# Kernel optimization log

Hardware: AMD Instinct MI355X
Metric: run time of the kernel (lower is better)

Reference implementation:

```python
import jax, jax.numpy as jnp
import numpy as np

B, T, N, D = 2, 256, 128, 512
H = 8
D_INNER, D_STATE, D_CONV, DT_RANK = 2 * D, 16, 4, D // 16  # mamba defaults
EPS = 1e-5


def setup_inputs() -> dict:
    key = jax.random.key(0)
    ks = iter(jax.random.split(key, 32))
    g = lambda shape, s=0.02: jax.random.normal(next(ks), shape, dtype=jnp.float32) * s
    return {
        "x": jax.random.normal(next(ks), (B, T, N, D), dtype=jnp.float32),
        "mha_in_w": g((3 * D, D)), "mha_in_b": jnp.zeros((3 * D,), jnp.float32),
        "mha_out_w": g((D, D)), "mha_out_b": jnp.zeros((D,), jnp.float32),
        "n1_w": jnp.ones((D,), jnp.float32),
        "n2_w": jnp.ones((D,), jnp.float32),
        "n3_w": jnp.ones((D,), jnp.float32),
        "m_in_w": g((2 * D_INNER, D)),
        "m_conv_w": g((D_INNER, 1, D_CONV), 0.1), "m_conv_b": jnp.zeros((D_INNER,), jnp.float32),
        "m_xproj_w": g((DT_RANK + 2 * D_STATE, D_INNER)),
        "m_dt_w": g((D_INNER, DT_RANK)), "m_dt_b": jnp.full((D_INNER,), -4.6, jnp.float32),
        "m_A_log": jnp.tile(jnp.log(jnp.arange(1, D_STATE + 1, dtype=jnp.float32)), (D_INNER, 1)),
        "m_D": jnp.ones((D_INNER,), jnp.float32),
        "m_out_w": g((D, D_INNER)),
        "mlp_w1": g((2 * D, D)), "mlp_b1": jnp.zeros((2 * D,), jnp.float32),
        "mlp_w2": g((D, 2 * D)), "mlp_b2": jnp.zeros((D,), jnp.float32),
    }


def rmsnorm(x, w):
    return x * jax.lax.rsqrt(jnp.mean(x * x, axis=-1, keepdims=True) + EPS) * w


def mha(x, in_w, in_b, out_w, out_b):
    # x: (Bt, N, D); torch nn.MultiheadAttention with batch_first=True
    Bt, n, d = x.shape
    dh = d // H
    qkv = x @ in_w.T + in_b
    q, k, v = jnp.split(qkv, 3, axis=-1)
    q = q.reshape(Bt, n, H, dh)
    k = k.reshape(Bt, n, H, dh)
    v = v.reshape(Bt, n, H, dh)
    att = jax.nn.softmax(jnp.einsum('bnhd,bmhd->bhnm', q, k) / jnp.sqrt(jnp.float32(dh)), axis=-1)
    o = jnp.einsum('bhnm,bmhd->bnhd', att, v).reshape(Bt, n, d)
    return o @ out_w.T + out_b


def mamba(x, in_w, conv_w, conv_b, xproj_w, dt_w, dt_b, A_log, Dp, out_w):
    # x: (Bm, L, D)  -- standard mamba_ssm Mamba block (expand=2, d_state=16, d_conv=4)
    Bm, L, _ = x.shape
    xz = x @ in_w.T                      # (Bm, L, 2*d_inner)
    xm, z = jnp.split(xz, 2, axis=-1)
    # causal depthwise conv1d along time
    xc = jnp.pad(xm.transpose(0, 2, 1), ((0, 0), (0, 0), (D_CONV - 1, 0)))
    xc = jax.lax.conv_general_dilated(xc, conv_w, (1,), 'VALID',
                                      dimension_numbers=('NCH', 'OIH', 'NCH'),
                                      feature_group_count=D_INNER)
    xm = jax.nn.silu(xc.transpose(0, 2, 1) + conv_b)   # (Bm, L, d_inner)
    x_dbl = xm @ xproj_w.T
    dt, Bs, Cs = jnp.split(x_dbl, [DT_RANK, DT_RANK + D_STATE], axis=-1)
    dt = jax.nn.softplus(dt @ dt_w.T + dt_b)           # (Bm, L, d_inner)
    A = -jnp.exp(A_log)                                # (d_inner, d_state)

    def step(h, inp):
        dt_t, B_t, C_t, u_t = inp                      # (Bm,d_in),(Bm,ds),(Bm,ds),(Bm,d_in)
        dA = jnp.exp(dt_t[:, :, None] * A)             # (Bm, d_inner, d_state)
        h = dA * h + (dt_t * u_t)[:, :, None] * B_t[:, None, :]
        y = jnp.einsum('bds,bs->bd', h, C_t)
        return h, y

    h0 = jnp.zeros((Bm, D_INNER, D_STATE), x.dtype)
    inputs = (dt.transpose(1, 0, 2), Bs.transpose(1, 0, 2),
              Cs.transpose(1, 0, 2), xm.transpose(1, 0, 2))
    _, ys = jax.lax.scan(step, h0, inputs)
    y = ys.transpose(1, 0, 2) + xm * Dp
    y = y * jax.nn.silu(z)
    return y @ out_w.T


def reference(x, mha_in_w, mha_in_b, mha_out_w, mha_out_b, n1_w, n2_w, n3_w,
              m_in_w, m_conv_w, m_conv_b, m_xproj_w, m_dt_w, m_dt_b, m_A_log, m_D, m_out_w,
              mlp_w1, mlp_b1, mlp_w2, mlp_b2):
    Bx, Tx, Nx, Dx = x.shape
    # spatial attention over regions
    xs = x.reshape(Bx * Tx, Nx, Dx)
    xs = rmsnorm(xs + mha(xs, mha_in_w, mha_in_b, mha_out_w, mha_out_b), n1_w)
    # temporal mamba over time
    xt = xs.reshape(Bx, Tx, Nx, Dx).transpose(0, 2, 1, 3).reshape(Bx * Nx, Tx, Dx)
    xt = rmsnorm(xt + mamba(xt, m_in_w, m_conv_w, m_conv_b, m_xproj_w,
                            m_dt_w, m_dt_b, m_A_log, m_D, m_out_w), n2_w)
    # MLP (1 hidden layer, width 2*D, ReLU)
    x3 = xt.reshape(Bx, Nx, Tx, Dx).transpose(0, 2, 1, 3)
    h = jax.nn.relu(x3 @ mlp_w1.T + mlp_b1) @ mlp_w2.T + mlp_b2
    return rmsnorm(x3 + h, n3_w)
```

## Files before the change

kernel.cpp:

```cpp
#include <hip/hip_runtime.h>

typedef unsigned short u16;
typedef unsigned int u32;
typedef __attribute__((ext_vector_type(8))) short short8;
typedef __attribute__((ext_vector_type(4))) float f32x4;

__device__ __forceinline__ float bf2f(u16 u){ union{u32 i; float f;} v; v.i=((u32)u)<<16; return v.f; }
__device__ __forceinline__ u16 f2bf(float f){ union{float f; u32 i;} v; v.f=f; u32 r=v.i+0x7FFFu+((v.i>>16)&1u); return (u16)(r>>16); }

__device__ __forceinline__ void glds16(const u16* g, u16* lds){
  __builtin_amdgcn_global_load_lds((const __attribute__((address_space(1))) u32*)g,
                                   (__attribute__((address_space(3))) u32*)lds, 16, 0, 0);
}

__global__ __launch_bounds__(256) void cvt_kernel(const float* __restrict__ src, u16* __restrict__ dst, int n4){
  int i = blockIdx.x*256 + threadIdx.x;
  if (i >= n4) return;
  float4 v = ((const float4*)src)[i];
  union { u16 o[4]; uint2 q; } t;
  t.o[0]=f2bf(v.x); t.o[1]=f2bf(v.y); t.o[2]=f2bf(v.z); t.o[3]=f2bf(v.w);
  ((uint2*)dst)[i] = t.q;
}

template<int BM, int BN, int EPI>
__global__ __launch_bounds__(256, 2) void gemm_bt_kernel(
    const u16* __restrict__ A, int lda,
    const u16* __restrict__ B,
    const float* __restrict__ bias,
    u16* __restrict__ C, int ldc,
    int N, int K)
{
  constexpr int RM = BM/32, RN = BN/32;
  constexpr int AI = BM/64, BI = BN/64;
  const int tid = threadIdx.x;
  const int wave = tid>>6, lane = tid&63;
  const int wm = wave>>1, wn = wave&1;
  const int lm = lane&15, quad = lane>>4;
  const int bm0 = blockIdx.x*BM, bn0 = blockIdx.y*BN;
  __shared__ __align__(16) u16 As[BM*32];
  __shared__ __align__(16) u16 Bs[BN*32];
  f32x4 acc[RM][RN] = {};
  const int vr = tid>>2, vc = (tid&3)<<3;
  for (int k0=0; k0<K; k0+=32){
    __syncthreads();
    #pragma unroll
    for (int i=0;i<AI;i++)
      glds16(A + (size_t)(bm0 + i*64 + vr)*lda + k0 + vc, &As[(i*256 + wave*64)*8]);
    #pragma unroll
    for (int i=0;i<BI;i++)
      glds16(B + (size_t)(bn0 + i*64 + vr)*K + k0 + vc, &Bs[(i*256 + wave*64)*8]);
    __syncthreads();
    short8 af[RM], bfr[RN];
    #pragma unroll
    for (int i=0;i<RM;i++) af[i] = *(const short8*)(&As[(wm*(BM/2)+i*16+lm)*32 + quad*8]);
    #pragma unroll
    for (int j=0;j<RN;j++) bfr[j] = *(const short8*)(&Bs[(wn*(BN/2)+j*16+lm)*32 + quad*8]);
    #pragma unroll
    for (int i=0;i<RM;i++)
      #pragma unroll
      for (int j=0;j<RN;j++)
        acc[i][j] = __builtin_amdgcn_mfma_f32_16x16x32_bf16(af[i], bfr[j], acc[i][j], 0,0,0);
  }
  #pragma unroll
  for (int j=0;j<RN;j++){
    int col = bn0 + wn*(BN/2) + j*16 + lm;
    float bv = 0.f;
    if (EPI >= 1) bv = bias[col];
    #pragma unroll
    for (int i=0;i<RM;i++){
      int r0 = bm0 + wm*(BM/2) + i*16 + quad*4;
      #pragma unroll
      for (int r=0;r<4;r++){
        float v = acc[i][j][r] + bv;
        if (EPI == 2) v = fmaxf(v, 0.f);
        if (EPI == 3) v = (v > 20.f) ? v : log1pf(__expf(v));
        C[(size_t)(r0+r)*ldc + col] = f2bf(v);
      }
    }
  }
}

__global__ __launch_bounds__(256, 2) void attn_kernel(const u16* __restrict__ qkv, u16* __restrict__ o)
{
  const int bb = blockIdx.x >> 3;
  const int hh = blockIdx.x & 7;
  const int tid = threadIdx.x;
  const int wave = tid>>6, lane = tid&63;
  const int lm = lane&15, quad = lane>>4;
  __shared__ union {
    struct { u16 Q[128][72]; u16 K[128][72]; } qk;
    u16 P[128][136];
  } sm;
  __shared__ __align__(16) u16 Vt[64][136];
  const size_t base = (size_t)bb*128*1536 + (size_t)hh*64;
  #pragma unroll
  for (int i=0;i<4;i++){
    int v = i*256 + tid;
    int r = v>>3, c = (v&7)<<3;
    *(uint4*)(&sm.qk.Q[r][c]) = *(const uint4*)(qkv + base + (size_t)r*1536 + c);
    *(uint4*)(&sm.qk.K[r][c]) = *(const uint4*)(qkv + base + 512 + (size_t)r*1536 + c);
    union { uint4 q; u16 u[8]; } vv;
    vv.q = *(const uint4*)(qkv + base + 1024 + (size_t)r*1536 + c);
    #pragma unroll
    for (int j=0;j<8;j++) Vt[c+j][r] = vv.u[j];
  }
  __syncthreads();
  f32x4 sa[2][8] = {};
  #pragma unroll
  for (int k0=0;k0<64;k0+=32){
    short8 af[2], bfr[8];
    #pragma unroll
    for (int i=0;i<2;i++) af[i] = *(const short8*)(&sm.qk.Q[wave*32+i*16+lm][k0+quad*8]);
    #pragma unroll
    for (int j=0;j<8;j++) bfr[j] = *(const short8*)(&sm.qk.K[j*16+lm][k0+quad*8]);
    #pragma unroll
    for (int i=0;i<2;i++)
      #pragma unroll
      for (int j=0;j<8;j++)
        sa[i][j] = __builtin_amdgcn_mfma_f32_16x16x32_bf16(af[i], bfr[j], sa[i][j], 0,0,0);
  }
  __syncthreads();
  #pragma unroll
  for (int i=0;i<2;i++){
    #pragma unroll
    for (int r=0;r<4;r++){
      float mx = -1e30f;
      #pragma unroll
      for (int j=0;j<8;j++) mx = fmaxf(mx, sa[i][j][r]);
      #pragma unroll
      for (int off=1; off<16; off<<=1) mx = fmaxf(mx, __shfl_xor(mx, off, 64));
      float pv[8]; float sum = 0.f;
      #pragma unroll
      for (int j=0;j<8;j++){ pv[j] = __expf((sa[i][j][r]-mx)*0.125f); sum += pv[j]; }
      #pragma unroll
      for (int off=1; off<16; off<<=1) sum += __shfl_xor(sum, off, 64);
      float inv = 1.f/sum;
      int row = wave*32 + i*16 + quad*4 + r;
      #pragma unroll
      for (int j=0;j<8;j++) sm.P[row][j*16+lm] = f2bf(pv[j]*inv);
    }
  }
  f32x4 oa[2][4] = {};
  #pragma unroll
  for (int k0=0;k0<128;k0+=32){
    short8 af[2], bfr[4];
    #pragma unroll
    for (int i=0;i<2;i++) af[i] = *(const short8*)(&sm.P[wave*32+i*16+lm][k0+quad*8]);
    #pragma unroll
    for (int j=0;j<4;j++) bfr[j] = *(const short8*)(&Vt[j*16+lm][k0+quad*8]);
    #pragma unroll
    for (int i=0;i<2;i++)
      #pragma unroll
      for (int j=0;j<4;j++)
        oa[i][j] = __builtin_amdgcn_mfma_f32_16x16x32_bf16(af[i], bfr[j], oa[i][j], 0,0,0);
  }
  #pragma unroll
  for (int i=0;i<2;i++)
    #pragma unroll
    for (int j=0;j<4;j++){
      int col = hh*64 + j*16 + lm;
      int r0 = wave*32 + i*16 + quad*4;
      #pragma unroll
      for (int r=0;r<4;r++)
        o[(size_t)(bb*128 + r0 + r)*512 + col] = f2bf(oa[i][j][r]);
    }
}

__global__ __launch_bounds__(256) void conv_silu_kernel(const u16* __restrict__ xc,
    const float* __restrict__ cw, const float* __restrict__ cb, u16* __restrict__ xm)
{
  int id = blockIdx.x*256 + threadIdx.x;
  int r = id >> 7, c8 = (id & 127) << 3;
  int t = r & 255;
  union { uint4 q; u16 u[8]; } rv[4];
  #pragma unroll
  for (int tap=0;tap<4;tap++){
    int ts = t - 3 + tap;
    if (ts >= 0) rv[tap].q = *(const uint4*)(xc + (size_t)(r-3+tap)*1024 + c8);
    else rv[tap].q = make_uint4(0,0,0,0);
  }
  union { uint4 q; u16 u[8]; } out;
  #pragma unroll
  for (int j=0;j<8;j++){
    float4 wj = ((const float4*)cw)[c8+j];
    float a = cb[c8+j];
    a += bf2f(rv[0].u[j])*wj.x + bf2f(rv[1].u[j])*wj.y + bf2f(rv[2].u[j])*wj.z + bf2f(rv[3].u[j])*wj.w;
    a = a / (1.f + __expf(-a));
    out.u[j] = f2bf(a);
  }
  *(uint4*)(xm + (size_t)r*1024 + c8) = out.q;
}

typedef union { uint4 q; u16 u[8]; } BC8;
__global__ __launch_bounds__(256) void scan_kernel(
    const u16* dtp, const u16* __restrict__ xm, const u16* __restrict__ xdbl,
    const u16* __restrict__ zp, const float* __restrict__ A_log, const float* __restrict__ Dp,
    u16* yp)
{
  int bm = blockIdx.x;
  int d = blockIdx.y*256 + threadIdx.x;
  float h[16];
  bool fast = true;
  #pragma unroll
  for (int s=0;s<16;s++){
    float a = __expf(A_log[d*16+s]);
    float tgt = (float)(s+1);
    fast = fast && (fabsf(a - tgt) <= 1e-4f*tgt);
    h[s] = 0.f;
  }
  float Dv = Dp[d];
  size_t rowbase = (size_t)bm*256;

  float dtb[2], ub[2], zvb[2];
  BC8 b0b[2], b1b[2], c0b[2], c1b[2];
  #pragma unroll
  for (int j=0;j<2;j++){
    size_t row = rowbase + j;
    dtb[j] = bf2f(dtp[row*1024 + d]);
    ub[j]  = bf2f(xm[row*1024 + d]);
    zvb[j] = bf2f(zp[row*1024 + d]);
    const u16* bc = xdbl + row*64;
    b0b[j].q = *(const uint4*)(bc+32); b1b[j].q = *(const uint4*)(bc+40);
    c0b[j].q = *(const uint4*)(bc+48); c1b[j].q = *(const uint4*)(bc+56);
  }
  #pragma unroll 2
  for (int t=0;t<256;t++){
    const int j = t & 1;
    const float dt = dtb[j], u = ub[j], z = zvb[j];
    const BC8 b0 = b0b[j], b1 = b1b[j], c0 = c0b[j], c1 = c1b[j];
    {
      size_t rown = rowbase + ((t+2) & 255);
      dtb[j] = bf2f(dtp[rown*1024 + d]);
      ub[j]  = bf2f(xm[rown*1024 + d]);
      zvb[j] = bf2f(zp[rown*1024 + d]);
      const u16* bcn = xdbl + rown*64;
      b0b[j].q = *(const uint4*)(bcn+32); b1b[j].q = *(const uint4*)(bcn+40);
      c0b[j].q = *(const uint4*)(bcn+48); c1b[j].q = *(const uint4*)(bcn+56);
    }
    const float du = dt*u;
    float ya[4] = {0.f, 0.f, 0.f, 0.f};
    if (fast){
      float e1 = __expf(-dt);
      float e2=e1*e1, e3=e2*e1, e4=e2*e2, e5=e4*e1, e6=e4*e2, e7=e4*e3, e8=e4*e4;
      float e9=e8*e1, e10=e8*e2, e11=e8*e3, e12=e8*e4, e13=e8*e5, e14=e8*e6, e15=e8*e7, e16=e8*e8;
      float pw[16] = {e1,e2,e3,e4,e5,e6,e7,e8,e9,e10,e11,e12,e13,e14,e15,e16};
      #pragma unroll
      for (int s=0;s<8;s++){
        h[s] = pw[s]*h[s] + du*bf2f(b0.u[s]);
        ya[s&3] += h[s]*bf2f(c0.u[s]);
      }
      #pragma unroll
      for (int s=0;s<8;s++){
        h[8+s] = pw[8+s]*h[8+s] + du*bf2f(b1.u[s]);
        ya[s&3] += h[8+s]*bf2f(c1.u[s]);
      }
    } else {
      #pragma unroll
      for (int s=0;s<8;s++){
        float As = -__expf(A_log[d*16+s]);
        h[s] = __expf(dt*As)*h[s] + du*bf2f(b0.u[s]);
        ya[s&3] += h[s]*bf2f(c0.u[s]);
      }
      #pragma unroll
      for (int s=0;s<8;s++){
        float As = -__expf(A_log[d*16+8+s]);
        h[8+s] = __expf(dt*As)*h[8+s] + du*bf2f(b1.u[s]);
        ya[s&3] += h[8+s]*bf2f(c1.u[s]);
      }
    }
    const float yv = (ya[0]+ya[1]) + (ya[2]+ya[3]);
    const float o = (yv + u*Dv) * (z / (1.f + __expf(-z)));
    yp[(rowbase + t)*1024 + d] = f2bf(o);
  }
}

template<int MODE>
__global__ __launch_bounds__(256) void transpose_kernel(const u16* __restrict__ in, u16* __restrict__ out){
  int id = blockIdx.x*256 + threadIdx.x;
  int row_out = id >> 6, v = (id & 63) << 3;
  int b = row_out >> 15, rem = row_out & 32767;
  int row_in;
  if (MODE == 0){ int n = rem >> 8, t = rem & 255; row_in = (b*256 + t)*128 + n; }
  else          { int t = rem >> 7, n = rem & 127; row_in = (b*128 + n)*256 + t; }
  *(uint4*)(out + (size_t)row_out*512 + v) = *(const uint4*)(in + (size_t)row_in*512 + v);
}

template<bool RES_F32, bool OUT_F32>
__global__ __launch_bounds__(256) void rmsnorm_kernel(const u16* mn,
    const void* res, const float* __restrict__ w, void* out)
{
  int row = blockIdx.x*4 + (threadIdx.x>>6);
  int lane = threadIdx.x & 63;
  size_t base = (size_t)row*512 + lane*8;
  union { uint4 q; u16 u[8]; } mv;
  mv.q = *(const uint4*)(mn + base);
  float vals[8];
  if (RES_F32){
    const float* rp = (const float*)res + base;
    float4 r0 = ((const float4*)rp)[0];
    float4 r1 = ((const float4*)rp)[1];
    float rr[8] = {r0.x,r0.y,r0.z,r0.w,r1.x,r1.y,r1.z,r1.w};
    #pragma unroll
    for (int j=0;j<8;j++) vals[j] = bf2f(mv.u[j]) + rr[j];
  } else {
    union { uint4 q; u16 u[8]; } rv;
    rv.q = *(const uint4*)((const u16*)res + base);
    #pragma unroll
    for (int j=0;j<8;j++) vals[j] = bf2f(mv.u[j]) + bf2f(rv.u[j]);
  }
  float ss = 0.f;
  #pragma unroll
  for (int j=0;j<8;j++) ss += vals[j]*vals[j];
  #pragma unroll
  for (int off=1; off<64; off<<=1) ss += __shfl_xor(ss, off, 64);
  float sc = rsqrtf(ss*(1.f/512.f) + 1e-5f);
  if (OUT_F32){
    float* op = (float*)out + base;
    float o[8];
    #pragma unroll
    for (int j=0;j<8;j++) o[j] = vals[j]*sc*w[lane*8+j];
    ((float4*)op)[0] = make_float4(o[0],o[1],o[2],o[3]);
    ((float4*)op)[1] = make_float4(o[4],o[5],o[6],o[7]);
  } else {
    union { uint4 q; u16 u[8]; } ov;
    #pragma unroll
    for (int j=0;j<8;j++) ov.u[j] = f2bf(vals[j]*sc*w[lane*8+j]);
    *(uint4*)((u16*)out + base) = ov.q;
  }
}

static size_t req_bytes(int NC){
  size_t R = 65536/NC;
  size_t regB = (R*2048 > 33554432ull) ? R*2048 : 33554432ull;
  return 2ull * (4194304ull + 33554432ull + regB + R*2560ull);
}

extern "C" void kernel_launch(void* const* d_in, const int* in_sizes, int n_in,
                              void* d_out, int out_size, void* d_ws, size_t ws_size,
                              hipStream_t stream)
{
  const float* x       = (const float*)d_in[0];
  const float* w_qkv_f = (const float*)d_in[1];
  const float* b_qkv   = (const float*)d_in[2];
  const float* w_out_f = (const float*)d_in[3];
  const float* b_out   = (const float*)d_in[4];
  const float* n1w     = (const float*)d_in[5];
  const float* n2w     = (const float*)d_in[6];
  const float* n3w     = (const float*)d_in[7];
  const float* w_min_f = (const float*)d_in[8];
  const float* convw   = (const float*)d_in[9];
  const float* convb   = (const float*)d_in[10];
  const float* w_xp_f  = (const float*)d_in[11];
  const float* w_dt_f  = (const float*)d_in[12];
  const float* b_dt    = (const float*)d_in[13];
  const float* A_log   = (const float*)d_in[14];
  const float* Dp      = (const float*)d_in[15];
  const float* w_mo_f  = (const float*)d_in[16];
  const float* w_1_f   = (const float*)d_in[17];
  const float* b_1     = (const float*)d_in[18];
  const float* w_2_f   = (const float*)d_in[19];
  const float* b_2     = (const float*)d_in[20];
  float* out = (float*)d_out;
  u16* wsu = (u16*)d_ws;

  int NC = 16;
  if      (ws_size >= req_bytes(1)) NC = 1;
  else if (ws_size >= req_bytes(2)) NC = 2;
  else if (ws_size >= req_bytes(4)) NC = 4;
  else if (ws_size >= req_bytes(8)) NC = 8;
  const size_t R = 65536/NC;

  u16* w_qkv = wsu;
  u16* w_o   = w_qkv + 786432;
  u16* w_mi  = w_o   + 262144;
  u16* w_xp  = w_mi  + 1048576;
  u16* w_dt  = w_xp  + 65536;
  u16* w_mo  = w_dt  + 32768;
  u16* w_1   = w_mo  + 524288;
  u16* w_2   = w_1   + 524288;
  u16* xt    = wsu + 4194304;
  const size_t baseB = 37748736;
  const size_t regB  = (R*2048 > 33554432ull) ? R*2048 : 33554432ull;
  const size_t baseC = baseB + regB;
  u16* o2    = wsu + baseB;
  u16* x3    = wsu + baseB;
  u16* zb    = wsu + baseB;
  u16* xmb   = wsu + baseB + R*1024;
  u16* xbf_c = wsu + baseC;
  u16* qkv_c = wsu + baseC + R*512;
  u16* oat_c = wsu + baseC + R*2048;
  u16* slab  = wsu + baseC;
  u16* xdbl_c= wsu + baseC + R*1024;
  u16* mo_c  = wsu + baseC + R*1088;
  u16* h1_c  = wsu + baseC;
  u16* h2_c  = wsu + baseC + R*1024;

  struct CV { const float* s; u16* d; int n; };
  const CV cvs[] = {
    {w_qkv_f, w_qkv, 786432}, {w_out_f, w_o, 262144}, {w_min_f, w_mi, 1048576},
    {w_xp_f, w_xp, 65536}, {w_dt_f, w_dt, 32768}, {w_mo_f, w_mo, 524288},
    {w_1_f, w_1, 524288}, {w_2_f, w_2, 524288},
  };
  for (int i = 0; i < 8; i++){
    int n4 = cvs[i].n / 4;
    cvt_kernel<<<(n4+255)/256, 256, 0, stream>>>(cvs[i].s, cvs[i].d, n4);
  }

  for (int c = 0; c < NC; c++){
    cvt_kernel<<<R/2, 256, 0, stream>>>(x + c*R*512, xbf_c, (int)(R*128));
    gemm_bt_kernel<128,128,1><<<dim3(R/128,12), 256, 0, stream>>>(xbf_c, 512, w_qkv, b_qkv, qkv_c, 1536, 1536, 512);
    attn_kernel<<<(R/128)*8, 256, 0, stream>>>(qkv_c, oat_c);
    gemm_bt_kernel<128,128,1><<<dim3(R/128,4), 256, 0, stream>>>(oat_c, 512, w_o, b_out, o2 + c*R*512, 512, 512, 512);
  }
  rmsnorm_kernel<true,false><<<16384, 256, 0, stream>>>(o2, x, n1w, o2);
  transpose_kernel<0><<<16384, 256, 0, stream>>>(o2, xt);

  for (int c = 0; c < NC; c++){
    const u16* xtc = xt + c*R*512;
    gemm_bt_kernel<128,128,0><<<dim3(R/128,8), 256, 0, stream>>>(xtc, 512, w_mi, nullptr, slab, 1024, 1024, 512);
    gemm_bt_kernel<128,128,0><<<dim3(R/128,8), 256, 0, stream>>>(xtc, 512, w_mi + 524288, nullptr, zb, 1024, 1024, 512);
    conv_silu_kernel<<<R/2, 256, 0, stream>>>(slab, convw, convb, xmb);
    gemm_bt_kernel<128,64,0><<<dim3(R/128,1), 256, 0, stream>>>(xmb, 1024, w_xp, nullptr, xdbl_c, 64, 64, 1024);
    gemm_bt_kernel<128,128,3><<<dim3(R/128,8), 256, 0, stream>>>(xdbl_c, 64, w_dt, b_dt, slab, 1024, 1024, 32);
    scan_kernel<<<dim3(R/256,4), 256, 0, stream>>>(slab, xmb, xdbl_c, zb, A_log, Dp, slab);
    gemm_bt_kernel<128,128,0><<<dim3(R/128,4), 256, 0, stream>>>(slab, 1024, w_mo, nullptr, mo_c, 512, 512, 1024);
    rmsnorm_kernel<false,false><<<R/4, 256, 0, stream>>>(mo_c, xtc, n2w, (void*)xtc);
  }
  transpose_kernel<1><<<16384, 256, 0, stream>>>(xt, x3);

  for (int c = 0; c < NC; c++){
    const u16* x3c = x3 + c*R*512;
    gemm_bt_kernel<128,128,2><<<dim3(R/128,8), 256, 0, stream>>>(x3c, 512, w_1, b_1, h1_c, 1024, 1024, 512);
    gemm_bt_kernel<128,128,1><<<dim3(R/128,4), 256, 0, stream>>>(h1_c, 1024, w_2, b_2, h2_c, 512, 512, 1024);
    rmsnorm_kernel<false,true><<<R/4, 256, 0, stream>>>(h2_c, x3c, n3w, out + c*R*512);
  }
}
```

Baseline: 1.913 ms.

## Fold final transpose into output rmsnorm scatter, tune gemm occupancy and xproj tile

```diff
diff --git a/kernel.cpp b/kernel.cpp
--- a/kernel.cpp
+++ b/kernel.cpp
@@ -23,7 +23,7 @@
 }
 
 template<int BM, int BN, int EPI>
-__global__ __launch_bounds__(256, 2) void gemm_bt_kernel(
+__global__ __launch_bounds__(256, 3) void gemm_bt_kernel(
     const u16* __restrict__ A, int lda,
     const u16* __restrict__ B,
     const float* __restrict__ bias,
@@ -274,20 +274,18 @@
   }
 }
 
-template<int MODE>
 __global__ __launch_bounds__(256) void transpose_kernel(const u16* __restrict__ in, u16* __restrict__ out){
   int id = blockIdx.x*256 + threadIdx.x;
   int row_out = id >> 6, v = (id & 63) << 3;
   int b = row_out >> 15, rem = row_out & 32767;
-  int row_in;
-  if (MODE == 0){ int n = rem >> 8, t = rem & 255; row_in = (b*256 + t)*128 + n; }
-  else          { int t = rem >> 7, n = rem & 127; row_in = (b*128 + n)*256 + t; }
+  int n = rem >> 8, t = rem & 255;
+  int row_in = (b*256 + t)*128 + n;
   *(uint4*)(out + (size_t)row_out*512 + v) = *(const uint4*)(in + (size_t)row_in*512 + v);
 }
 
-template<bool RES_F32, bool OUT_F32>
+template<bool RES_F32, bool OUT_F32, bool PERM>
 __global__ __launch_bounds__(256) void rmsnorm_kernel(const u16* mn,
-    const void* res, const float* __restrict__ w, void* out)
+    const void* res, const float* __restrict__ w, void* out, int rowoff)
 {
   int row = blockIdx.x*4 + (threadIdx.x>>6);
   int lane = threadIdx.x & 63;
@@ -314,8 +312,14 @@
   #pragma unroll
   for (int off=1; off<64; off<<=1) ss += __shfl_xor(ss, off, 64);
   float sc = rsqrtf(ss*(1.f/512.f) + 1e-5f);
+  size_t obase = base;
+  if (PERM){
+    int g = row + rowoff;
+    int p = ((g>>15)<<15) | ((g&255)<<7) | ((g>>8)&127);
+    obase = (size_t)p*512 + lane*8;
+  }
   if (OUT_F32){
-    float* op = (float*)out + base;
+    float* op = (float*)out + obase;
     float o[8];
     #pragma unroll
     for (int j=0;j<8;j++) o[j] = vals[j]*sc*w[lane*8+j];
@@ -325,7 +329,7 @@
     union { uint4 q; u16 u[8]; } ov;
     #pragma unroll
     for (int j=0;j<8;j++) ov.u[j] = f2bf(vals[j]*sc*w[lane*8+j]);
-    *(uint4*)((u16*)out + base) = ov.q;
+    *(uint4*)((u16*)out + obase) = ov.q;
   }
 }
 
@@ -383,7 +387,6 @@
   const size_t regB  = (R*2048 > 33554432ull) ? R*2048 : 33554432ull;
   const size_t baseC = baseB + regB;
   u16* o2    = wsu + baseB;
-  u16* x3    = wsu + baseB;
   u16* zb    = wsu + baseB;
   u16* xmb   = wsu + baseB + R*1024;
   u16* xbf_c = wsu + baseC;
@@ -412,26 +415,25 @@
     attn_kernel<<<(R/128)*8, 256, 0, stream>>>(qkv_c, oat_c);
     gemm_bt_kernel<128,128,1><<<dim3(R/128,4), 256, 0, stream>>>(oat_c, 512, w_o, b_out, o2 + c*R*512, 512, 512, 512);
   }
-  rmsnorm_kernel<true,false><<<16384, 256, 0, stream>>>(o2, x, n1w, o2);
-  transpose_kernel<0><<<16384, 256, 0, stream>>>(o2, xt);
+  rmsnorm_kernel<true,false,false><<<16384, 256, 0, stream>>>(o2, x, n1w, o2, 0);
+  transpose_kernel<<<16384, 256, 0, stream>>>(o2, xt);
 
   for (int c = 0; c < NC; c++){
     const u16* xtc = xt + c*R*512;
     gemm_bt_kernel<128,128,0><<<dim3(R/128,8), 256, 0, stream>>>(xtc, 512, w_mi, nullptr, slab, 1024, 1024, 512);
     gemm_bt_kernel<128,128,0><<<dim3(R/128,8), 256, 0, stream>>>(xtc, 512, w_mi + 524288, nullptr, zb, 1024, 1024, 512);
     conv_silu_kernel<<<R/2, 256, 0, stream>>>(slab, convw, convb, xmb);
-    gemm_bt_kernel<128,64,0><<<dim3(R/128,1), 256, 0, stream>>>(xmb, 1024, w_xp, nullptr, xdbl_c, 64, 64, 1024);
+    gemm_bt_kernel<64,64,0><<<dim3(R/64,1), 256, 0, stream>>>(xmb, 1024, w_xp, nullptr, xdbl_c, 64, 64, 1024);
     gemm_bt_kernel<128,128,3><<<dim3(R/128,8), 256, 0, stream>>>(xdbl_c, 64, w_dt, b_dt, slab, 1024, 1024, 32);
     scan_kernel<<<dim3(R/256,4), 256, 0, stream>>>(slab, xmb, xdbl_c, zb, A_log, Dp, slab);
     gemm_bt_kernel<128,128,0><<<dim3(R/128,4), 256, 0, stream>>>(slab, 1024, w_mo, nullptr, mo_c, 512, 512, 1024);
-    rmsnorm_kernel<false,false><<<R/4, 256, 0, stream>>>(mo_c, xtc, n2w, (void*)xtc);
-  }
-  transpose_kernel<1><<<16384, 256, 0, stream>>>(xt, x3);
+    rmsnorm_kernel<false,false,false><<<R/4, 256, 0, stream>>>(mo_c, xtc, n2w, (void*)xtc, 0);
+  }
 
   for (int c = 0; c < NC; c++){
-    const u16* x3c = x3 + c*R*512;
+    const u16* x3c = xt + c*R*512;
     gemm_bt_kernel<128,128,2><<<dim3(R/128,8), 256, 0, stream>>>(x3c, 512, w_1, b_1, h1_c, 1024, 1024, 512);
     gemm_bt_kernel<128,128,1><<<dim3(R/128,4), 256, 0, stream>>>(h1_c, 1024, w_2, b_2, h2_c, 512, 512, 1024);
-    rmsnorm_kernel<false,true><<<R/4, 256, 0, stream>>>(h2_c, x3c, n3w, out + c*R*512);
-  }
-}
+    rmsnorm_kernel<false,true,true><<<R/4, 256, 0, stream>>>(h2_c, x3c, n3w, out, (int)(c*R));
+  }
+}
```

New measurement: 1.864 ms. -2.6%, faster.
